# Optimization experiments

Hardware: AMD Instinct MI355X
Metric: run time of the kernel (lower is better)

## Reference

```python
import jax, jax.numpy as jnp
import numpy as np

DIM = 768
NUM_HEADS = 12
HEAD_DIM = DIM // NUM_HEADS
SCALE = HEAD_DIM ** -0.5


def setup_inputs() -> dict:
    key = jax.random.key(0)
    k1, k2, k3, k4 = jax.random.split(key, 4)
    B, N = 4, 2048
    x = jax.random.normal(k1, (B, N, DIM), dtype=jnp.float32)
    w_qkv = jax.random.normal(k2, (DIM, 3 * DIM), dtype=jnp.float32) * (DIM ** -0.5)
    w_proj = jax.random.normal(k3, (DIM, DIM), dtype=jnp.float32) * (DIM ** -0.5)
    b_proj = jax.random.normal(k4, (DIM,), dtype=jnp.float32) * 0.02
    return {"x": x, "w_qkv": w_qkv, "w_proj": w_proj, "b_proj": b_proj}


def reference(x, w_qkv, w_proj, b_proj):
    B, N, C = x.shape
    H, Dh = NUM_HEADS, HEAD_DIM
    # qkv: [B, N, 3, H, Dh] -> q,k,v each [B, H, N, Dh]
    qkv = (x @ w_qkv).reshape(B, N, 3, H, Dh)
    q = qkv[:, :, 0].transpose(0, 2, 1, 3) * SCALE
    k = qkv[:, :, 1].transpose(0, 2, 1, 3)
    v = qkv[:, :, 2].transpose(0, 2, 1, 3)
    attn = jax.nn.softmax(jnp.einsum('bhnd,bhmd->bhnm', q, k), axis=-1)
    out = jnp.einsum('bhnm,bhmd->bhnd', attn, v)  # [B, H, N, Dh]
    out = out.transpose(0, 2, 1, 3).reshape(B, N, C)
    return out @ w_proj + b_proj
```

## Files before the change

kernel.cpp:

```cpp
#include <hip/hip_runtime.h>

typedef unsigned short u16;
typedef __bf16 bf16x8 __attribute__((ext_vector_type(8)));
typedef __bf16 bf16x4 __attribute__((ext_vector_type(4)));
typedef short s16x4 __attribute__((ext_vector_type(4)));
typedef float f32x4 __attribute__((ext_vector_type(4)));
typedef _Float16 f16x4 __attribute__((ext_vector_type(4)));
typedef unsigned short u16x8 __attribute__((ext_vector_type(8)));
typedef unsigned short u16x4 __attribute__((ext_vector_type(4)));

__device__ __forceinline__ u16 f2bf(float x) {
  union { float f; unsigned u; } c; c.f = x;
  unsigned r = c.u + 0x7FFFu + ((c.u >> 16) & 1u);
  return (u16)(r >> 16);
}

__device__ __forceinline__ void glds16(const void* g, void* s) {
  __builtin_amdgcn_global_load_lds(
      (const __attribute__((address_space(1))) unsigned int*)g,
      (__attribute__((address_space(3))) unsigned int*)s, 16, 0, 0);
}

__global__ __launch_bounds__(256) void k_cast_x(const float* __restrict__ x,
                                                u16* __restrict__ o) {
  int i = blockIdx.x * 256 + threadIdx.x;
  const f32x4* xp = (const f32x4*)x + (size_t)i * 2;
  f32x4 a = xp[0], b = xp[1];
  u16x8 r;
  r[0] = f2bf(a[0]); r[1] = f2bf(a[1]); r[2] = f2bf(a[2]); r[3] = f2bf(a[3]);
  r[4] = f2bf(b[0]); r[5] = f2bf(b[1]); r[6] = f2bf(b[2]); r[7] = f2bf(b[3]);
  *((u16x8*)o + i) = r;
}

__global__ __launch_bounds__(256) void k_transpose_w(const float* __restrict__ src,
                                                     u16* __restrict__ dst,
                                                     int K, int Nn) {
  __shared__ float tile[64 * 68];
  int tid = threadIdx.x;
  int n0 = blockIdx.x * 64, k0 = blockIdx.y * 64;
  int rr = tid >> 4, cc = tid & 15;
#pragma unroll
  for (int r = 0; r < 4; ++r) {
    int k = r * 16 + rr;
    f32x4 v = *(const f32x4*)(src + (size_t)(k0 + k) * Nn + n0 + cc * 4);
    *(f32x4*)(tile + k * 68 + cc * 4) = v;
  }
  __syncthreads();
#pragma unroll
  for (int r = 0; r < 4; ++r) {
    int n = r * 16 + rr;
    u16x4 o;
#pragma unroll
    for (int j = 0; j < 4; ++j) o[j] = f2bf(tile[(cc * 4 + j) * 68 + n]);
    *(u16x4*)(dst + (size_t)(n0 + n) * K + k0 + cc * 4) = o;
  }
}

template <int BM, int N, bool PROJ>
__global__ __launch_bounds__(256) void k_gemm(const u16* __restrict__ A,
                                              const u16* __restrict__ Bt,
                                              u16* __restrict__ Co,
                                              float* __restrict__ Cf,
                                              const float* __restrict__ bias,
                                              u16* __restrict__ vt) {
  const int K = 768;
  const int FI = BM / 32;
  __shared__ u16 lA[BM * 64];
  __shared__ u16 lB[128 * 64];
  const int tid = threadIdx.x;
  const int wave = tid >> 6, lane = tid & 63;
  const int lr = lane & 15, lq = lane >> 4;
  const int m0 = blockIdx.x * BM, n0 = blockIdx.y * 128;
  const int wr = (wave >> 1) * (BM / 2), wc = (wave & 1) * 64;
  f32x4 acc[FI][4] = {};
  for (int k0 = 0; k0 < K; k0 += 64) {
#pragma unroll
    for (int r = 0; r < BM / 32; ++r) {
      int ch = r * 256 + tid;
      int mm = ch >> 3, cs = ch & 7;
      glds16(A + (size_t)(m0 + mm) * K + k0 + ((cs ^ (mm & 7)) << 3), lA + ch * 8);
    }
#pragma unroll
    for (int r = 0; r < 4; ++r) {
      int ch = r * 256 + tid;
      int mm = ch >> 3, cs = ch & 7;
      glds16(Bt + (size_t)(n0 + mm) * K + k0 + ((cs ^ (mm & 7)) << 3), lB + ch * 8);
    }
    __syncthreads();
#pragma unroll
    for (int ks = 0; ks < 2; ++ks) {
      bf16x8 af[FI], bfr[4];
#pragma unroll
      for (int f = 0; f < FI; ++f) {
        int ma = wr + f * 16 + lr;
        af[f] = *(const bf16x8*)(lA + (ma * 8 + ((ks * 4 + lq) ^ (ma & 7))) * 8);
      }
#pragma unroll
      for (int f = 0; f < 4; ++f) {
        int nb = wc + f * 16 + lr;
        bfr[f] = *(const bf16x8*)(lB + (nb * 8 + ((ks * 4 + lq) ^ (nb & 7))) * 8);
      }
#pragma unroll
      for (int fi = 0; fi < FI; ++fi)
#pragma unroll
        for (int fj = 0; fj < 4; ++fj)
          acc[fi][fj] = __builtin_amdgcn_mfma_f32_16x16x32_bf16(
              af[fi], bfr[fj], acc[fi][fj], 0, 0, 0);
    }
    __syncthreads();
  }
#pragma unroll
  for (int fi = 0; fi < FI; ++fi) {
#pragma unroll
    for (int fj = 0; fj < 4; ++fj) {
      int row = m0 + wr + fi * 16 + lq * 4;
      int col = n0 + wc + fj * 16 + lr;
      if constexpr (PROJ) {
        float bv = bias[col];
#pragma unroll
        for (int g = 0; g < 4; ++g)
          Cf[(size_t)(row + g) * N + col] = acc[fi][fj][g] + bv;
      } else {
        if (n0 + wc >= 1536) {
          int hh = (col - 1536) >> 6, dd = col & 63;
          u16x4 o;
#pragma unroll
          for (int g = 0; g < 4; ++g) o[g] = f2bf(acc[fi][fj][g]);
          *(u16x4*)(vt + (((size_t)(row >> 11) * 12 + hh) * 64 + dd) * 2048 +
                    (row & 2047)) = o;
        } else {
          const float qs = 0.18033688011112042f;
          float s = (col < 768) ? qs : 1.0f;
#pragma unroll
          for (int g = 0; g < 4; ++g)
            Co[(size_t)(row + g) * N + col] = f2bf(acc[fi][fj][g] * s);
        }
      }
    }
  }
}

__global__ __launch_bounds__(256) void k_attn(const u16* __restrict__ qkv,
                                              const u16* __restrict__ vt,
                                              u16* __restrict__ p0,
                                              u16* __restrict__ p1,
                                              float* __restrict__ Lp) {
  const int SEQ = 2048, C3 = 2304;
  __shared__ u16 lK[128 * 64];
  __shared__ u16 lV[64 * 128];
  const int tid = threadIdx.x;
  const int wave = tid >> 6, lane = tid & 63;
  const int lr = lane & 15, lq = lane >> 4;
  const int n0 = blockIdx.x * 128;
  const int bh = blockIdx.y;
  const int jh = blockIdx.z;
  const int b = bh / 12, h = bh % 12;
  const u16* qb = qkv + (size_t)b * SEQ * C3 + h * 64;
  const u16* kb = qb + 768;
  const u16* vb = vt + (size_t)bh * 64 * SEQ;

#pragma unroll
  for (int r = 0; r < 4; ++r) {
    int ch = r * 256 + tid;
    int mm = ch >> 3, cs = ch & 7;
    glds16(qb + (size_t)(n0 + mm) * C3 + ((cs ^ (mm & 7)) << 3), lK + ch * 8);
  }
  __syncthreads();
  bf16x8 qf[2][2];
#pragma unroll
  for (int rf = 0; rf < 2; ++rf) {
    int mq = wave * 32 + rf * 16 + lr;
#pragma unroll
    for (int ks = 0; ks < 2; ++ks)
      qf[rf][ks] = *(const bf16x8*)(lK + (mq * 8 + ((ks * 4 + lq) ^ (mq & 7))) * 8);
  }

  f32x4 O[2][4] = {};
  float lsum[2] = {0.f, 0.f};

  for (int tt = 0; tt < 8; ++tt) {
    int j0 = jh * 1024 + tt * 128;
    __syncthreads();
#pragma unroll
    for (int r = 0; r < 4; ++r) {
      int ch = r * 256 + tid;
      int mm = ch >> 3, cs = ch & 7;
      glds16(kb + (size_t)(j0 + mm) * C3 + ((cs ^ (mm & 7)) << 3), lK + ch * 8);
      int dd = ch >> 4, ct = ch & 15;
      glds16(vb + (size_t)dd * SEQ + j0 + ((ct ^ (dd & 7)) << 3), lV + ch * 8);
    }
    __syncthreads();

#pragma unroll
    for (int half = 0; half < 2; ++half) {
      f32x4 S[4][2];
#pragma unroll
      for (int cf = 0; cf < 4; ++cf)
#pragma unroll
        for (int rf = 0; rf < 2; ++rf)
          S[cf][rf] = (f32x4){-8.f, -8.f, -8.f, -8.f};
#pragma unroll
      for (int ks = 0; ks < 2; ++ks) {
#pragma unroll
        for (int cf = 0; cf < 4; ++cf) {
          int j = (half * 4 + cf) * 16 + lr;
          bf16x8 kf = *(const bf16x8*)(lK + (j * 8 + ((ks * 4 + lq) ^ (j & 7))) * 8);
#pragma unroll
          for (int rf = 0; rf < 2; ++rf)
            S[cf][rf] = __builtin_amdgcn_mfma_f32_16x16x32_bf16(
                kf, qf[rf][ks], S[cf][rf], 0, 0, 0);
        }
      }
      union PU { bf16x4 b; s16x4 s; } P[4][2];
#pragma unroll
      for (int cf = 0; cf < 4; ++cf)
#pragma unroll
        for (int rf = 0; rf < 2; ++rf) {
          f32x4 p;
#pragma unroll
          for (int g = 0; g < 4; ++g) p[g] = __builtin_amdgcn_exp2f(S[cf][rf][g]);
          lsum[rf] += (p[0] + p[1]) + (p[2] + p[3]);
          bf16x4 pb;
#pragma unroll
          for (int g = 0; g < 4; ++g) pb[g] = (__bf16)p[g];
          P[cf][rf].b = pb;
        }
#pragma unroll
      for (int cf = 0; cf < 4; ++cf) {
        int c2 = (half * 4 + cf) * 2 + (lq >> 1);
#pragma unroll
        for (int df = 0; df < 4; ++df) {
          int d = df * 16 + lr;
          s16x4 vf = *(const s16x4*)(lV + d * 128 + ((c2 ^ (d & 7)) << 3) + (lq & 1) * 4);
#pragma unroll
          for (int rf = 0; rf < 2; ++rf)
            O[rf][df] = __builtin_amdgcn_mfma_f32_16x16x16bf16_1k(
                vf, P[cf][rf].s, O[rf][df], 0, 0, 0);
        }
      }
    }
  }

  u16* pd = jh ? p1 : p0;
  float* Lb = Lp + (size_t)(jh * 48 + bh) * 2048;
#pragma unroll
  for (int rf = 0; rf < 2; ++rf) {
    float s = lsum[rf];
    s += __shfl_xor(s, 16);
    s += __shfl_xor(s, 32);
    int rowl = n0 + wave * 32 + rf * 16 + lr;
    if (lq == 0) Lb[rowl] = s;
    size_t row = (size_t)b * SEQ + rowl;
#pragma unroll
    for (int df = 0; df < 4; ++df) {
      union { f16x4 h; u16x4 u; } o;
#pragma unroll
      for (int g = 0; g < 4; ++g) o.h[g] = (_Float16)O[rf][df][g];
      *(u16x4*)(pd + row * 768 + h * 64 + df * 16 + lq * 4) = o.u;
    }
  }
}

__global__ __launch_bounds__(256) void k_merge(const u16* __restrict__ p0,
                                               u16* __restrict__ p1,
                                               const float* __restrict__ Lp) {
  int t = blockIdx.x * 256 + threadIdx.x;
  int row = t / 192, c4 = (t % 192) * 4;
  int hh = c4 >> 6;
  int bh = (row >> 11) * 12 + hh, rowl = row & 2047;
  float l = Lp[(size_t)bh * 2048 + rowl] + Lp[(size_t)(48 + bh) * 2048 + rowl];
  float inv = 1.0f / l;
  size_t off = (size_t)row * 768 + c4;
  union { f16x4 h; u16x4 u; } a, bb;
  a.u = *(const u16x4*)(p0 + off);
  bb.u = *(const u16x4*)(p1 + off);
  u16x4 o;
#pragma unroll
  for (int g = 0; g < 4; ++g)
    o[g] = f2bf(((float)a.h[g] + (float)bb.h[g]) * inv);
  *(u16x4*)(p1 + off) = o;
}

extern "C" void kernel_launch(void* const* d_in, const int* in_sizes, int n_in,
                              void* d_out, int out_size, void* d_ws, size_t ws_size,
                              hipStream_t stream) {
  const float* x = (const float*)d_in[0];
  const float* w_qkv = (const float*)d_in[1];
  const float* w_proj = (const float*)d_in[2];
  const float* b_proj = (const float*)d_in[3];
  float* out = (float*)d_out;
  char* ws = (char*)d_ws;
  u16* x_bf    = (u16*)(ws);
  u16* wqkv_t  = (u16*)(ws + 12582912);
  u16* wproj_t = (u16*)(ws + 16121856);
  u16* qkv     = (u16*)(ws + 17301504);
  u16* vt      = (u16*)(ws + 55050240);
  u16* aout    = (u16*)(ws + 67633152);
  float* Lp    = (float*)wqkv_t;

  k_cast_x<<<3072, 256, 0, stream>>>(x, x_bf);
  k_transpose_w<<<dim3(36, 12), 256, 0, stream>>>(w_qkv, wqkv_t, 768, 2304);
  k_transpose_w<<<dim3(12, 12), 256, 0, stream>>>(w_proj, wproj_t, 768, 768);
  k_gemm<128, 2304, false><<<dim3(64, 18), 256, 0, stream>>>(x_bf, wqkv_t, qkv,
                                                             nullptr, nullptr, vt);
  k_attn<<<dim3(16, 48, 2), 256, 0, stream>>>(qkv, vt, x_bf, aout, Lp);
  k_merge<<<6144, 256, 0, stream>>>(x_bf, aout, Lp);
  k_gemm<64, 768, true><<<dim3(128, 6), 256, 0, stream>>>(aout, wproj_t, nullptr,
                                                          out, b_proj, nullptr);
}
```

Before: 241.2 us.

## Merge preprocessing kernels and compute softmax row sums via MFMA

Combines the x cast and both weight transposes into one kernel launch using block-index ranges, removing two launches and their gaps. In attention, the softmax denominator is accumulated with an extra MFMA against a ones vector instead of VALU adds plus cross-lane shuffles. It also seeds the first QK MFMA directly with the bias constant and adds a minimum-occupancy hint to launch bounds. The sum now uses bf16-rounded probabilities and adds matrix-core work, and the occupancy hint may constrain registers.

```diff
diff --git a/kernel.cpp b/kernel.cpp
--- a/kernel.cpp
+++ b/kernel.cpp
@@ -21,23 +21,31 @@
       (__attribute__((address_space(3))) unsigned int*)s, 16, 0, 0);
 }
 
-__global__ __launch_bounds__(256) void k_cast_x(const float* __restrict__ x,
-                                                u16* __restrict__ o) {
-  int i = blockIdx.x * 256 + threadIdx.x;
-  const f32x4* xp = (const f32x4*)x + (size_t)i * 2;
-  f32x4 a = xp[0], b = xp[1];
-  u16x8 r;
-  r[0] = f2bf(a[0]); r[1] = f2bf(a[1]); r[2] = f2bf(a[2]); r[3] = f2bf(a[3]);
-  r[4] = f2bf(b[0]); r[5] = f2bf(b[1]); r[6] = f2bf(b[2]); r[7] = f2bf(b[3]);
-  *((u16x8*)o + i) = r;
-}
-
-__global__ __launch_bounds__(256) void k_transpose_w(const float* __restrict__ src,
-                                                     u16* __restrict__ dst,
-                                                     int K, int Nn) {
+__global__ __launch_bounds__(256) void k_pre(const float* __restrict__ x,
+                                             u16* __restrict__ xbf,
+                                             const float* __restrict__ wq,
+                                             u16* __restrict__ wqt,
+                                             const float* __restrict__ wp,
+                                             u16* __restrict__ wpt) {
   __shared__ float tile[64 * 68];
+  int bx = blockIdx.x;
   int tid = threadIdx.x;
-  int n0 = blockIdx.x * 64, k0 = blockIdx.y * 64;
+  if (bx < 3072) {
+    int i = bx * 256 + tid;
+    const f32x4* xp = (const f32x4*)x + (size_t)i * 2;
+    f32x4 a = xp[0], b = xp[1];
+    u16x8 r;
+    r[0] = f2bf(a[0]); r[1] = f2bf(a[1]); r[2] = f2bf(a[2]); r[3] = f2bf(a[3]);
+    r[4] = f2bf(b[0]); r[5] = f2bf(b[1]); r[6] = f2bf(b[2]); r[7] = f2bf(b[3]);
+    *((u16x8*)xbf + i) = r;
+    return;
+  }
+  const float* src; u16* dst; int Nn, n0, k0;
+  const int K = 768;
+  if (bx < 3504) { int b2 = bx - 3072; src = wq; dst = wqt; Nn = 2304;
+                   n0 = (b2 % 36) * 64; k0 = (b2 / 36) * 64; }
+  else           { int b2 = bx - 3504; src = wp; dst = wpt; Nn = 768;
+                   n0 = (b2 % 12) * 64; k0 = (b2 / 12) * 64; }
   int rr = tid >> 4, cc = tid & 15;
 #pragma unroll
   for (int r = 0; r < 4; ++r) {
@@ -140,11 +148,11 @@
   }
 }
 
-__global__ __launch_bounds__(256) void k_attn(const u16* __restrict__ qkv,
-                                              const u16* __restrict__ vt,
-                                              u16* __restrict__ p0,
-                                              u16* __restrict__ p1,
-                                              float* __restrict__ Lp) {
+__global__ __launch_bounds__(256, 4) void k_attn(const u16* __restrict__ qkv,
+                                                 const u16* __restrict__ vt,
+                                                 u16* __restrict__ p0,
+                                                 u16* __restrict__ p1,
+                                                 float* __restrict__ Lp) {
   const int SEQ = 2048, C3 = 2304;
   __shared__ u16 lK[128 * 64];
   __shared__ u16 lV[64 * 128];
@@ -175,8 +183,10 @@
       qf[rf][ks] = *(const bf16x8*)(lK + (mq * 8 + ((ks * 4 + lq) ^ (mq & 7))) * 8);
   }
 
+  const f32x4 biasC = {-8.f, -8.f, -8.f, -8.f};
+  const s16x4 onesA = {16256, 16256, 16256, 16256};
   f32x4 O[2][4] = {};
-  float lsum[2] = {0.f, 0.f};
+  f32x4 L5[2] = {};
 
   for (int tt = 0; tt < 8; ++tt) {
     int j0 = jh * 1024 + tt * 128;
@@ -195,39 +205,41 @@
     for (int half = 0; half < 2; ++half) {
       f32x4 S[4][2];
 #pragma unroll
+      for (int cf = 0; cf < 4; ++cf) {
+        int j = (half * 4 + cf) * 16 + lr;
+        bf16x8 kf = *(const bf16x8*)(lK + (j * 8 + (lq ^ (j & 7))) * 8);
+#pragma unroll
+        for (int rf = 0; rf < 2; ++rf)
+          S[cf][rf] = __builtin_amdgcn_mfma_f32_16x16x32_bf16(
+              kf, qf[rf][0], biasC, 0, 0, 0);
+      }
+#pragma unroll
+      for (int cf = 0; cf < 4; ++cf) {
+        int j = (half * 4 + cf) * 16 + lr;
+        bf16x8 kf = *(const bf16x8*)(lK + (j * 8 + ((4 + lq) ^ (j & 7))) * 8);
+#pragma unroll
+        for (int rf = 0; rf < 2; ++rf)
+          S[cf][rf] = __builtin_amdgcn_mfma_f32_16x16x32_bf16(
+              kf, qf[rf][1], S[cf][rf], 0, 0, 0);
+      }
+      union PU { bf16x4 b; s16x4 s; } P[4][2];
+#pragma unroll
       for (int cf = 0; cf < 4; ++cf)
 #pragma unroll
-        for (int rf = 0; rf < 2; ++rf)
-          S[cf][rf] = (f32x4){-8.f, -8.f, -8.f, -8.f};
-#pragma unroll
-      for (int ks = 0; ks < 2; ++ks) {
-#pragma unroll
-        for (int cf = 0; cf < 4; ++cf) {
-          int j = (half * 4 + cf) * 16 + lr;
-          bf16x8 kf = *(const bf16x8*)(lK + (j * 8 + ((ks * 4 + lq) ^ (j & 7))) * 8);
-#pragma unroll
-          for (int rf = 0; rf < 2; ++rf)
-            S[cf][rf] = __builtin_amdgcn_mfma_f32_16x16x32_bf16(
-                kf, qf[rf][ks], S[cf][rf], 0, 0, 0);
-        }
-      }
-      union PU { bf16x4 b; s16x4 s; } P[4][2];
-#pragma unroll
-      for (int cf = 0; cf < 4; ++cf)
-#pragma unroll
         for (int rf = 0; rf < 2; ++rf) {
-          f32x4 p;
-#pragma unroll
-          for (int g = 0; g < 4; ++g) p[g] = __builtin_amdgcn_exp2f(S[cf][rf][g]);
-          lsum[rf] += (p[0] + p[1]) + (p[2] + p[3]);
           bf16x4 pb;
 #pragma unroll
-          for (int g = 0; g < 4; ++g) pb[g] = (__bf16)p[g];
+          for (int g = 0; g < 4; ++g)
+            pb[g] = (__bf16)__builtin_amdgcn_exp2f(S[cf][rf][g]);
           P[cf][rf].b = pb;
         }
 #pragma unroll
       for (int cf = 0; cf < 4; ++cf) {
         int c2 = (half * 4 + cf) * 2 + (lq >> 1);
+#pragma unroll
+        for (int rf = 0; rf < 2; ++rf)
+          L5[rf] = __builtin_amdgcn_mfma_f32_16x16x16bf16_1k(
+              onesA, P[cf][rf].s, L5[rf], 0, 0, 0);
 #pragma unroll
         for (int df = 0; df < 4; ++df) {
           int d = df * 16 + lr;
@@ -245,11 +257,8 @@
   float* Lb = Lp + (size_t)(jh * 48 + bh) * 2048;
 #pragma unroll
   for (int rf = 0; rf < 2; ++rf) {
-    float s = lsum[rf];
-    s += __shfl_xor(s, 16);
-    s += __shfl_xor(s, 32);
     int rowl = n0 + wave * 32 + rf * 16 + lr;
-    if (lq == 0) Lb[rowl] = s;
+    if (lq == 0) Lb[rowl] = L5[rf][0];
     size_t row = (size_t)b * SEQ + rowl;
 #pragma unroll
     for (int df = 0; df < 4; ++df) {
@@ -298,9 +307,7 @@
   u16* aout    = (u16*)(ws + 67633152);
   float* Lp    = (float*)wqkv_t;
 
-  k_cast_x<<<3072, 256, 0, stream>>>(x, x_bf);
-  k_transpose_w<<<dim3(36, 12), 256, 0, stream>>>(w_qkv, wqkv_t, 768, 2304);
-  k_transpose_w<<<dim3(12, 12), 256, 0, stream>>>(w_proj, wproj_t, 768, 768);
+  k_pre<<<3648, 256, 0, stream>>>(x, x_bf, w_qkv, wqkv_t, w_proj, wproj_t);
   k_gemm<128, 2304, false><<<dim3(64, 18), 256, 0, stream>>>(x_bf, wqkv_t, qkv,
                                                              nullptr, nullptr, vt);
   k_attn<<<dim3(16, 48, 2), 256, 0, stream>>>(qkv, vt, x_bf, aout, Lp);
```

Result: no change. 239.0 us (-0.9%).
